# Kernel optimization log

Measured on AMD Instinct MI355X. Metric: run time of the kernel, lower is better.

## Reference

```python
import jax, jax.numpy as jnp
import numpy as np

N = 50000      # nodes
E = 600000     # edges
D_IN = 128     # node_dim
D = 128        # out_channels
T = 4          # num_node_types
R = 4          # num_edge_types
L = 2          # num_layers
C = 8          # num_class
G = 512        # graphs in batch


def setup_inputs() -> dict:
    key = jax.random.key(0)
    ks = jax.random.split(key, 12)
    s = 0.05
    x = jax.random.normal(ks[0], (N, D_IN), jnp.float32)
    node_type = jax.random.randint(ks[1], (N,), 0, T)
    edge_index = jax.random.randint(ks[2], (2, E), 0, N)
    edge_type = jax.random.randint(ks[3], (E,), 0, R)
    batch = jnp.sort(jax.random.randint(ks[4], (N,), 0, G))
    # learned params
    W_het = jax.random.normal(ks[5], (T, D_IN, D), jnp.float32) * s
    b_het = jnp.zeros((T, D), jnp.float32)
    conv_W = jax.random.normal(ks[6], (L, R, D, D), jnp.float32) * s
    conv_b = jnp.zeros((L, R, D), jnp.float32)
    fuse_W = jax.random.normal(ks[7], (R * D, D), jnp.float32) * s
    fuse_b = jnp.zeros((D,), jnp.float32)
    cls_W = jax.random.normal(ks[8], (D, C), jnp.float32) * s
    cls_b = jnp.zeros((C,), jnp.float32)
    return dict(x=x, W_het=W_het, b_het=b_het, conv_W=conv_W, conv_b=conv_b,
                fuse_W=fuse_W, fuse_b=fuse_b, cls_W=cls_W, cls_b=cls_b,
                node_type=node_type, edge_index=edge_index, edge_type=edge_type,
                batch=batch)


def reference(x, W_het, b_het, conv_W, conv_b, fuse_W, fuse_b, cls_W, cls_b,
              node_type, edge_index, edge_type, batch):
    n = x.shape[0]
    # HeteroLinear: per-node-type linear. Compute all T projections then select.
    x_all = jnp.einsum('nd,tdo->tno', x, W_het)          # [T, N, D]
    h = x_all[node_type, jnp.arange(n)] + b_het[node_type]
    src, dst = edge_index[0], edge_index[1]
    for l in range(L):
        hs = h[src]                                       # [E, D] gather once per layer
        outs = []
        for r in range(R):
            # edges of relation r only (boolean mask == per-relation edge filtering)
            m = hs @ conv_W[l, r]                         # [E, D]
            m = m * (edge_type == r).astype(m.dtype)[:, None]
            agg = jax.ops.segment_sum(m, dst, num_segments=n)  # scatter-add to dst
            outs.append(agg + conv_b[l, r])
        h = jax.nn.relu(jnp.concatenate(outs, axis=1) @ fuse_W + fuse_b)
    # global mean pool over graphs
    counts = jax.ops.segment_sum(jnp.ones((n,), h.dtype), batch, num_segments=G)
    emb = jax.ops.segment_sum(h, batch, num_segments=G) / jnp.maximum(counts, 1.0)[:, None]
    logits = emb @ cls_W + cls_b
    return emb, logits
```

## Files before the change

### kernel.cpp

```cpp
#include <hip/hip_runtime.h>

#define N_NODES 50000
#define N_EDGES 600000
#define DIM     128
#define RR      4
#define LL      2
#define GG      512
#define CC      8
#define NCB     196
#define EC      (N_EDGES / 4)
#define FB      ((EC + 255) / 256)
#define TB      ((N_NODES + 255) / 256)
#define NBH     ((N_NODES + 63) / 64)
#define CB      (1026 + 3125)

typedef short bf16x8 __attribute__((ext_vector_type(8)));
typedef float f32x4  __attribute__((ext_vector_type(4)));

__device__ __forceinline__ float bf16_to_f(unsigned short u) {
    return __uint_as_float(((unsigned int)u) << 16);
}
__device__ __forceinline__ unsigned short f_to_bf16(float f) {
    unsigned int u = __float_as_uint(f);
    u += 0x7FFFu + ((u >> 16) & 1u);
    return (unsigned short)(u >> 16);
}
__device__ __forceinline__ float loadf(const void* p, long i, int isbf) {
    if (isbf) return bf16_to_f(((const unsigned short*)p)[i]);
    return ((const float*)p)[i];
}
__device__ __forceinline__ void storef(void* p, long i, float v, int isbf) {
    if (isbf) ((unsigned short*)p)[i] = f_to_bf16(v);
    else      ((float*)p)[i] = v;
}

__global__ void cg_init(const unsigned int* __restrict__ xw, int* __restrict__ flag,
                        int* __restrict__ chist_tb) {
    __shared__ int cnt;
    int tid = threadIdx.x;
    if (tid < NCB + 16) chist_tb[tid] = 0;
    if (tid == 0) cnt = 0;
    __syncthreads();
    unsigned int w = xw[tid];
    unsigned int e = (w >> 7) & 0xFFu;
    atomicAdd(&cnt, (e >= 110u && e <= 133u) ? 1 : 0);
    __syncthreads();
    if (tid == 0) *flag = (cnt >= 128) ? 1 : 0;
}

__global__ void cg_hist_canon(const int* __restrict__ edge_index, const int* __restrict__ node_type,
                              int* __restrict__ chist, int* __restrict__ tb,
                              const void* __restrict__ x,
                              const void* __restrict__ W_het, const void* __restrict__ b_het,
                              const void* __restrict__ conv_W, const void* __restrict__ fuse_W,
                              const void* __restrict__ conv_b, const void* __restrict__ fuse_b,
                              const int* __restrict__ flagp,
                              unsigned short* __restrict__ xb, unsigned short* __restrict__ Wt,
                              float* __restrict__ bhf,
                              unsigned short* __restrict__ M2t, float* __restrict__ cvec) {
    __shared__ float s[256];
    int bk = blockIdx.x;
    int tid = threadIdx.x;
    if (bk < FB) {
        __shared__ int lh[NCB];
        __shared__ int loc[4];
        for (int i = tid; i < NCB; i += 256) lh[i] = 0;
        if (tid < 4) loc[tid] = 0;
        __syncthreads();
        int t = bk * 256 + tid;
        if (t < EC) {
#pragma unroll
            for (int k = 0; k < 4; k++) {
                int d = edge_index[N_EDGES + t + k * EC];
                atomicAdd(&lh[d >> 8], 1);
            }
        }
        if (t < N_NODES) atomicAdd(&loc[node_type[t]], 1);
        __syncthreads();
        for (int i = tid; i < NCB; i += 256)
            if (lh[i]) atomicAdd(&chist[i], lh[i]);
        if (tid < 4 && loc[tid]) atomicAdd(&tb[tid], loc[tid]);
        return;
    }
    int b = bk - FB;
    int isbf = *flagp;
    if (b < 512) {
        int lr = b >> 6;
        int d  = (b & 63) * 2 + (tid >> 7);
        int r  = lr & 3;
        int o  = tid & 127;
        float acc = 0.0f;
        for (int k = 0; k < DIM; k++) {
            acc += loadf(conv_W, (long)(lr * DIM + d) * DIM + k, isbf)
                 * loadf(fuse_W, (long)(r * DIM + k) * DIM + o, isbf);
        }
        M2t[((long)lr * DIM + o) * DIM + d] = f_to_bf16(acc);
    } else if (b < 768) {
        int bc = b - 512;
        int l  = bc >> 7;
        int o  = bc & 127;
        float part = 0.0f;
        for (int rk = tid; rk < RR * DIM; rk += 256) {
            part += loadf(conv_b, (long)l * RR * DIM + rk, isbf)
                  * loadf(fuse_W, (long)rk * DIM + o, isbf);
        }
        s[tid] = part;
        __syncthreads();
        for (int off = 128; off > 0; off >>= 1) {
            if (tid < off) s[tid] += s[tid + off];
            __syncthreads();
        }
        if (tid == 0) cvec[bc] = s[0] + loadf(fuse_b, o, isbf);
    } else if (b < 1024) {
        int pair = (b - 768) * 2 + (tid >> 7);
        int t = pair >> 7;
        int o = pair & 127;
        int d = tid & 127;
        float v = loadf(W_het, ((long)t * DIM + d) * DIM + o, isbf);
        Wt[((long)t * DIM + o) * DIM + d] = f_to_bf16(v);
    } else if (b < 1026) {
        int idx = (b - 1024) * 256 + tid;
        if (idx < 4 * DIM) bhf[idx] = loadf(b_het, idx, isbf);
    } else {
        long i = ((long)(b - 1026) * 256 + tid) * 8;
        if (i >= (long)N_NODES * DIM) return;
        if (isbf) {
            *(uint4*)(xb + i) = *(const uint4*)((const unsigned short*)x + i);
        } else {
            const float* xf = (const float*)x + i;
            float4 f0 = *(const float4*)xf;
            float4 f1 = *(const float4*)(xf + 4);
            uint4 o;
            o.x = (unsigned int)f_to_bf16(f0.x) | ((unsigned int)f_to_bf16(f0.y) << 16);
            o.y = (unsigned int)f_to_bf16(f0.z) | ((unsigned int)f_to_bf16(f0.w) << 16);
            o.z = (unsigned int)f_to_bf16(f1.x) | ((unsigned int)f_to_bf16(f1.y) << 16);
            o.w = (unsigned int)f_to_bf16(f1.z) | ((unsigned int)f_to_bf16(f1.w) << 16);
            *(uint4*)(xb + i) = o;
        }
    }
}

__global__ void cg_scan196(const int* __restrict__ chist, int* __restrict__ blockoff,
                           int* __restrict__ ccursor, int* __restrict__ tb) {
    __shared__ int s[256];
    int tid = threadIdx.x;
    int v = (tid < NCB) ? chist[tid] : 0;
    s[tid] = v;
    __syncthreads();
    for (int off = 1; off < 256; off <<= 1) {
        int a = (tid >= off) ? s[tid - off] : 0;
        __syncthreads();
        s[tid] += a;
        __syncthreads();
    }
    if (tid < NCB) {
        int e = s[tid] - v;
        blockoff[tid] = e;
        ccursor[tid]  = e;
    }
    if (tid == 0) {
        int run = 0;
        for (int t = 0; t < 4; t++) {
            tb[8 + t] = run;
            tb[4 + t] = run;
            run += tb[t];
        }
        tb[12] = run;
    }
}

__global__ void cg_tfill(const int* __restrict__ node_type, int* __restrict__ tb,
                         int* __restrict__ tlist) {
    __shared__ int lcur[4];
    __shared__ int lbase[4];
    int tid = threadIdx.x;
    if (tid < 4) lcur[tid] = 0;
    __syncthreads();
    int n = blockIdx.x * 256 + tid;
    int slot = -1, t = 0;
    if (n < N_NODES) {
        t = node_type[n];
        slot = atomicAdd(&lcur[t], 1);
    }
    __syncthreads();
    if (tid < 4) lbase[tid] = atomicAdd(&tb[4 + tid], lcur[tid]);
    __syncthreads();
    if (n < N_NODES) tlist[lbase[t] + slot] = n;
}

#define APAD 136

__global__ void cg_sortA_hetero(const int* __restrict__ edge_index, const int* __restrict__ edge_type,
                                int* __restrict__ ccursor, int2* __restrict__ tmp2,
                                const unsigned short* __restrict__ xb,
                                const unsigned short* __restrict__ Wt,
                                const float* __restrict__ bhf,
                                const int* __restrict__ tlist, const int* __restrict__ tb,
                                unsigned short* __restrict__ h) {
    __shared__ unsigned short a_lds[64][APAD];
    __shared__ unsigned short b_lds[DIM][APAD];
    int bk = blockIdx.x;
    int tx = threadIdx.x;
    if (bk < FB) {
        __shared__ int lhist[NCB];
        __shared__ int lbase[NCB];
        for (int i = tx; i < NCB; i += 256) lhist[i] = 0;
        __syncthreads();
        int t = bk * 256 + tx;
        int d[4], cb[4], ls[4], pl[4];
        bool act = (t < EC);
        if (act) {
#pragma unroll
            for (int k = 0; k < 4; k++) {
                int e = t + k * EC;
                d[k]  = edge_index[N_EDGES + e];
                pl[k] = (edge_index[e] << 2) | edge_type[e];
                cb[k] = d[k] >> 8;
                ls[k] = atomicAdd(&lhist[cb[k]], 1);
            }
        }
        __syncthreads();
        for (int i = tx; i < NCB; i += 256)
            lbase[i] = lhist[i] ? atomicAdd(&ccursor[i], lhist[i]) : 0;
        __syncthreads();
        if (act) {
#pragma unroll
            for (int k = 0; k < 4; k++) {
                int pos = lbase[cb[k]] + ls[k];
                tmp2[pos] = make_int2(pl[k], d[k]);
            }
        }
        return;
    }
    int bb = bk - FB;
    int t    = bb / NBH;
    int nblk = bb - t * NBH;
    int rows_base = tb[8 + t] + nblk * 64;
    int rend = tb[8 + t + 1];
    if (rows_base >= rend) return;
    const unsigned short* Wsrc = Wt + (long)t * DIM * DIM;
    for (int i = tx; i < 2048; i += 256) {
        uint4 w = *(const uint4*)(Wsrc + i * 8);
        int o = i >> 4, d2 = (i & 15) * 8;
        *(uint4*)&b_lds[o][d2] = w;
    }
    for (int i = tx; i < 1024; i += 256) {
        int row = i >> 4, seg = (i & 15) * 8;
        int gr = rows_base + row;
        uint4 w = make_uint4(0u, 0u, 0u, 0u);
        if (gr < rend) {
            int n = tlist[gr];
            w = *(const uint4*)(xb + (long)n * DIM + seg);
        }
        *(uint4*)&a_lds[row][seg] = w;
    }
    __syncthreads();
    int wv = tx >> 6, lane = tx & 63;
    int m16 = lane & 15, quad = lane >> 4;
    f32x4 acc[8];
#pragma unroll
    for (int c = 0; c < 8; c++) acc[c] = (f32x4){0.f, 0.f, 0.f, 0.f};
    for (int ks = 0; ks < 4; ks++) {
        int koff = ks * 32 + quad * 8;
        bf16x8 af = *(const bf16x8*)(const void*)&a_lds[wv * 16 + m16][koff];
#pragma unroll
        for (int c = 0; c < 8; c++) {
            bf16x8 bfr = *(const bf16x8*)(const void*)&b_lds[c * 16 + m16][koff];
            acc[c] = __builtin_amdgcn_mfma_f32_16x16x32_bf16(af, bfr, acc[c], 0, 0, 0);
        }
    }
    __syncthreads();
#pragma unroll
    for (int c = 0; c < 8; c++) {
#pragma unroll
        for (int i = 0; i < 4; i++) {
            int row = wv * 16 + quad * 4 + i;
            int col = c * 16 + m16;
            a_lds[row][col] = f_to_bf16(acc[c][i] + bhf[t * DIM + col]);
        }
    }
    __syncthreads();
    for (int i = tx; i < 1024; i += 256) {
        int row = i >> 4, seg = (i & 15) * 8;
        int gr = rows_base + row;
        if (gr < rend) {
            int n = tlist[gr];
            *(uint4*)(h + (long)n * DIM + seg) = *(const uint4*)&a_lds[row][seg];
        }
    }
}

__global__ void cg_sortB_pgemm(const int2* __restrict__ tmp2, const int* __restrict__ blockoff,
                               int* __restrict__ rowptr, int* __restrict__ eidx,
                               const unsigned short* __restrict__ h,
                               const unsigned short* __restrict__ M2t,
                               unsigned short* __restrict__ P) {
    __shared__ unsigned short a_lds[64][APAD];
    __shared__ unsigned short b_lds[DIM][APAD];
    int bk = blockIdx.x;
    int tx = threadIdx.x;
    if (bk < NCB) {
        __shared__ int lcnt[256];
        __shared__ int lscan[256];
        __shared__ int lcur[256];
        lcnt[tx] = 0;
        int base = blockoff[bk];
        int endp = (bk + 1 < NCB) ? blockoff[bk + 1] : N_EDGES;
        int cnt = endp - base;
        __syncthreads();
        for (int i = tx; i < cnt; i += 256)
            atomicAdd(&lcnt[tmp2[base + i].y & 255], 1);
        __syncthreads();
        int v = lcnt[tx];
        lscan[tx] = v;
        __syncthreads();
        for (int off = 1; off < 256; off <<= 1) {
            int a = (tx >= off) ? lscan[tx - off] : 0;
            __syncthreads();
            lscan[tx] += a;
            __syncthreads();
        }
        int start = base + lscan[tx] - v;
        lcur[tx] = start;
        int n = bk * 256 + tx;
        if (n < N_NODES) rowptr[n] = start;
        __syncthreads();
        for (int i = tx; i < cnt; i += 256) {
            int2 e = tmp2[base + i];
            int pos = atomicAdd(&lcur[e.y & 255], 1);
            eidx[pos] = e.x;
        }
        return;
    }
    int bb = bk - NCB;
    int r    = bb / NBH;
    int nblk = bb - r * NBH;
    int n0 = nblk * 64;
    const unsigned short* Bsrc = M2t + (long)r * DIM * DIM;
    for (int i = tx; i < 2048; i += 256) {
        uint4 w = *(const uint4*)(Bsrc + i * 8);
        int o = i >> 4, d = (i & 15) * 8;
        *(uint4*)&b_lds[o][d] = w;
    }
    for (int i = tx; i < 1024; i += 256) {
        int row = i >> 4, seg = (i & 15) * 8;
        int n = n0 + row;
        uint4 w = make_uint4(0u, 0u, 0u, 0u);
        if (n < N_NODES) w = *(const uint4*)(h + (long)n * DIM + seg);
        *(uint4*)&a_lds[row][seg] = w;
    }
    __syncthreads();
    int wv = tx >> 6, lane = tx & 63;
    int m16 = lane & 15, quad = lane >> 4;
    f32x4 acc[8];
#pragma unroll
    for (int c = 0; c < 8; c++) acc[c] = (f32x4){0.f, 0.f, 0.f, 0.f};
    for (int ks = 0; ks < 4; ks++) {
        int koff = ks * 32 + quad * 8;
        bf16x8 af = *(const bf16x8*)(const void*)&a_lds[wv * 16 + m16][koff];
#pragma unroll
        for (int c = 0; c < 8; c++) {
            bf16x8 bfr = *(const bf16x8*)(const void*)&b_lds[c * 16 + m16][koff];
            acc[c] = __builtin_amdgcn_mfma_f32_16x16x32_bf16(af, bfr, acc[c], 0, 0, 0);
        }
    }
    __syncthreads();
#pragma unroll
    for (int c = 0; c < 8; c++) {
#pragma unroll
        for (int i = 0; i < 4; i++) {
            int row = wv * 16 + quad * 4 + i;
            int col = c * 16 + m16;
            a_lds[row][col] = f_to_bf16(acc[c][i]);
        }
    }
    __syncthreads();
    for (int i = tx; i < 1024; i += 256) {
        int row = i >> 4, seg = (i & 15) * 8;
        int n = n0 + row;
        if (n < N_NODES)
            *(uint4*)(P + (long)n * (RR * DIM) + r * DIM + seg) = *(const uint4*)&a_lds[row][seg];
    }
}

__global__ void cg_pgemm_mfma(const unsigned short* __restrict__ h,
                              const unsigned short* __restrict__ M2t, int l,
                              unsigned short* __restrict__ P) {
    int r  = blockIdx.y;
    int n0 = blockIdx.x * 64;
    __shared__ unsigned short a_lds[64][APAD];
    __shared__ unsigned short b_lds[DIM][APAD];
    int tx = threadIdx.x;
    const unsigned short* Bsrc = M2t + (long)(l * RR + r) * DIM * DIM;
    for (int i = tx; i < 2048; i += 256) {
        uint4 w = *(const uint4*)(Bsrc + i * 8);
        int o = i >> 4, d = (i & 15) * 8;
        *(uint4*)&b_lds[o][d] = w;
    }
    for (int i = tx; i < 1024; i += 256) {
        int row = i >> 4, seg = (i & 15) * 8;
        int n = n0 + row;
        uint4 w = make_uint4(0u, 0u, 0u, 0u);
        if (n < N_NODES) w = *(const uint4*)(h + (long)n * DIM + seg);
        *(uint4*)&a_lds[row][seg] = w;
    }
    __syncthreads();
    int wv = tx >> 6, lane = tx & 63;
    int m16 = lane & 15, quad = lane >> 4;
    f32x4 acc[8];
#pragma unroll
    for (int c = 0; c < 8; c++) acc[c] = (f32x4){0.f, 0.f, 0.f, 0.f};
    for (int ks = 0; ks < 4; ks++) {
        int koff = ks * 32 + quad * 8;
        bf16x8 af = *(const bf16x8*)(const void*)&a_lds[wv * 16 + m16][koff];
#pragma unroll
        for (int c = 0; c < 8; c++) {
            bf16x8 bfr = *(const bf16x8*)(const void*)&b_lds[c * 16 + m16][koff];
            acc[c] = __builtin_amdgcn_mfma_f32_16x16x32_bf16(af, bfr, acc[c], 0, 0, 0);
        }
    }
    __syncthreads();
#pragma unroll
    for (int c = 0; c < 8; c++) {
#pragma unroll
        for (int i = 0; i < 4; i++) {
            int row = wv * 16 + quad * 4 + i;
            int col = c * 16 + m16;
            a_lds[row][col] = f_to_bf16(acc[c][i]);
        }
    }
    __syncthreads();
    for (int i = tx; i < 1024; i += 256) {
        int row = i >> 4, seg = (i & 15) * 8;
        int n = n0 + row;
        if (n < N_NODES)
            *(uint4*)(P + (long)n * (RR * DIM) + r * DIM + seg) = *(const uint4*)&a_lds[row][seg];
    }
}

__global__ void cg_gather4(const unsigned short* __restrict__ P, const int* __restrict__ rowptr,
                           const int* __restrict__ eidx, const float* __restrict__ cv,
                           unsigned short* __restrict__ hout) {
    int wid  = (blockIdx.x * 256 + threadIdx.x) >> 6;
    int lane = threadIdx.x & 63;
    if (wid >= N_NODES) return;
    int eg = lane >> 4;
    int ol = lane & 15;
    int start = rowptr[wid];
    int end   = (wid + 1 < N_NODES) ? rowptr[wid + 1] : N_EDGES;
    float a[8] = {0.f, 0.f, 0.f, 0.f, 0.f, 0.f, 0.f, 0.f};
    int j = start + eg;
    for (; j + 4 < end; j += 8) {
        int v0 = eidx[j];
        int v1 = eidx[j + 4];
        const uint4 w0 = *(const uint4*)(P + (long)(v0 >> 2) * (RR * DIM) + (v0 & 3) * DIM + ol * 8);
        const uint4 w1 = *(const uint4*)(P + (long)(v1 >> 2) * (RR * DIM) + (v1 & 3) * DIM + ol * 8);
        a[0] += bf16_to_f((unsigned short)(w0.x & 0xFFFFu)) + bf16_to_f((unsigned short)(w1.x & 0xFFFFu));
        a[1] += bf16_to_f((unsigned short)(w0.x >> 16))     + bf16_to_f((unsigned short)(w1.x >> 16));
        a[2] += bf16_to_f((unsigned short)(w0.y & 0xFFFFu)) + bf16_to_f((unsigned short)(w1.y & 0xFFFFu));
        a[3] += bf16_to_f((unsigned short)(w0.y >> 16))     + bf16_to_f((unsigned short)(w1.y >> 16));
        a[4] += bf16_to_f((unsigned short)(w0.z & 0xFFFFu)) + bf16_to_f((unsigned short)(w1.z & 0xFFFFu));
        a[5] += bf16_to_f((unsigned short)(w0.z >> 16))     + bf16_to_f((unsigned short)(w1.z >> 16));
        a[6] += bf16_to_f((unsigned short)(w0.w & 0xFFFFu)) + bf16_to_f((unsigned short)(w1.w & 0xFFFFu));
        a[7] += bf16_to_f((unsigned short)(w0.w >> 16))     + bf16_to_f((unsigned short)(w1.w >> 16));
    }
    if (j < end) {
        int v = eidx[j];
        const uint4 w = *(const uint4*)(P + (long)(v >> 2) * (RR * DIM) + (v & 3) * DIM + ol * 8);
        a[0] += bf16_to_f((unsigned short)(w.x & 0xFFFFu));
        a[1] += bf16_to_f((unsigned short)(w.x >> 16));
        a[2] += bf16_to_f((unsigned short)(w.y & 0xFFFFu));
        a[3] += bf16_to_f((unsigned short)(w.y >> 16));
        a[4] += bf16_to_f((unsigned short)(w.z & 0xFFFFu));
        a[5] += bf16_to_f((unsigned short)(w.z >> 16));
        a[6] += bf16_to_f((unsigned short)(w.w & 0xFFFFu));
        a[7] += bf16_to_f((unsigned short)(w.w >> 16));
    }
#pragma unroll
    for (int i = 0; i < 8; i++) {
        a[i] += __shfl_xor(a[i], 16);
        a[i] += __shfl_xor(a[i], 32);
    }
    if (eg == 0) {
        int o0 = ol * 8;
        float v[8];
#pragma unroll
        for (int i = 0; i < 8; i++) {
            float s = a[i] + cv[o0 + i];
            v[i] = s > 0.0f ? s : 0.0f;
        }
        uint4 o4;
        o4.x = (unsigned int)f_to_bf16(v[0]) | ((unsigned int)f_to_bf16(v[1]) << 16);
        o4.y = (unsigned int)f_to_bf16(v[2]) | ((unsigned int)f_to_bf16(v[3]) << 16);
        o4.z = (unsigned int)f_to_bf16(v[4]) | ((unsigned int)f_to_bf16(v[5]) << 16);
        o4.w = (unsigned int)f_to_bf16(v[6]) | ((unsigned int)f_to_bf16(v[7]) << 16);
        *(uint4*)(hout + (long)wid * DIM + o0) = o4;
    }
}

__global__ void cg_pool_logits(const unsigned short* __restrict__ h, const int* __restrict__ batch,
                               const void* __restrict__ cls_W, const void* __restrict__ cls_b,
                               const int* __restrict__ flagp, void* __restrict__ out) {
    __shared__ float acc_s[4][DIM];
    __shared__ float emb_s[DIM];
    int g   = blockIdx.x;
    int tid = threadIdx.x;
    int wv  = tid >> 6;
    int lane = tid & 63;
    int sub = lane >> 4;
    int ol  = lane & 15;
    int isbf = *flagp;
    int lo = 0, hi = N_NODES;
    while (lo < hi) { int mid = (lo + hi) >> 1; if (batch[mid] < g) lo = mid + 1; else hi = mid; }
    int start = lo;
    hi = N_NODES;
    while (lo < hi) { int mid = (lo + hi) >> 1; if (batch[mid] < g + 1) lo = mid + 1; else hi = mid; }
    int end = lo;
    float a[8] = {0.f, 0.f, 0.f, 0.f, 0.f, 0.f, 0.f, 0.f};
    for (int n = start + wv * 4 + sub; n < end; n += 16) {
        uint4 w = *(const uint4*)(h + (long)n * DIM + ol * 8);
        a[0] += bf16_to_f((unsigned short)(w.x & 0xFFFFu));
        a[1] += bf16_to_f((unsigned short)(w.x >> 16));
        a[2] += bf16_to_f((unsigned short)(w.y & 0xFFFFu));
        a[3] += bf16_to_f((unsigned short)(w.y >> 16));
        a[4] += bf16_to_f((unsigned short)(w.z & 0xFFFFu));
        a[5] += bf16_to_f((unsigned short)(w.z >> 16));
        a[6] += bf16_to_f((unsigned short)(w.w & 0xFFFFu));
        a[7] += bf16_to_f((unsigned short)(w.w >> 16));
    }
#pragma unroll
    for (int i = 0; i < 8; i++) {
        a[i] += __shfl_xor(a[i], 16);
        a[i] += __shfl_xor(a[i], 32);
    }
    if (sub == 0) {
#pragma unroll
        for (int i = 0; i < 8; i++) acc_s[wv][ol * 8 + i] = a[i];
    }
    __syncthreads();
    int cnt = end - start;
    float inv = 1.0f / (float)(cnt > 1 ? cnt : 1);
    if (tid < DIM) {
        float e = (acc_s[0][tid] + acc_s[1][tid] + acc_s[2][tid] + acc_s[3][tid]) * inv;
        emb_s[tid] = e;
        storef(out, (long)g * DIM + tid, e, isbf);
    }
    __syncthreads();
    if (tid < 128) {
        int c  = tid >> 4;
        int kk = tid & 15;
        float p = 0.0f;
#pragma unroll
        for (int k = kk * 8; k < kk * 8 + 8; k++)
            p += emb_s[k] * loadf(cls_W, (long)k * CC + c, isbf);
        p += __shfl_xor(p, 1);
        p += __shfl_xor(p, 2);
        p += __shfl_xor(p, 4);
        p += __shfl_xor(p, 8);
        if (kk == 0)
            storef(out, (long)GG * DIM + g * CC + c, p + loadf(cls_b, c, isbf), isbf);
    }
}

extern "C" void kernel_launch(void* const* d_in, const int* in_sizes, int n_in,
                              void* d_out, int out_size, void* d_ws, size_t ws_size,
                              hipStream_t stream) {
    const void* x      = d_in[0];
    const void* W_het  = d_in[1];
    const void* b_het  = d_in[2];
    const void* conv_W = d_in[3];
    const void* conv_b = d_in[4];
    const void* fuse_W = d_in[5];
    const void* fuse_b = d_in[6];
    const void* cls_W  = d_in[7];
    const void* cls_b  = d_in[8];
    const int* node_type  = (const int*)d_in[9];
    const int* edge_index = (const int*)d_in[10];
    const int* edge_type  = (const int*)d_in[11];
    const int* batch      = (const int*)d_in[12];

    char* base = (char*)d_ws;
    unsigned short* hbf      = (unsigned short*)(base + 0);
    unsigned short* P        = (unsigned short*)(base + 12800000);
    unsigned short* xb       = (unsigned short*)(base + 64000000);
    unsigned short* Wt       = (unsigned short*)(base + 76800000);
    float*          bhf      = (float*)(base + 76931072);
    unsigned short* M2t      = (unsigned short*)(base + 76933120);
    float*          cvec     = (float*)(base + 77195264);
    int*            rowptr   = (int*)(base + 77196288);
    int*            chist    = (int*)(base + 77396320);
    int*            tb       = chist + NCB;
    int*            blockoff = (int*)(base + 77397408);
    int*            ccursor  = (int*)(base + 77398432);
    int*            eidx     = (int*)(base + 77399456);
    int*            tlist    = (int*)(base + 79799456);
    int*            flag     = (int*)(base + 79999456);
    int2*           tmp2     = (int2*)(base + 79999472);

    cg_init<<<1, 256, 0, stream>>>((const unsigned int*)x, flag, chist);
    cg_hist_canon<<<FB + CB, 256, 0, stream>>>(edge_index, node_type, chist, tb,
                                               x, W_het, b_het, conv_W, fuse_W,
                                               conv_b, fuse_b, flag,
                                               xb, Wt, bhf, M2t, cvec);
    cg_scan196<<<1, 256, 0, stream>>>(chist, blockoff, ccursor, tb);
    cg_tfill<<<TB, 256, 0, stream>>>(node_type, tb, tlist);
    cg_sortA_hetero<<<FB + 4 * NBH, 256, 0, stream>>>(edge_index, edge_type, ccursor, tmp2,
                                                      xb, Wt, bhf, tlist, tb, hbf);
    cg_sortB_pgemm<<<NCB + 4 * NBH, 256, 0, stream>>>(tmp2, blockoff, rowptr, eidx,
                                                      hbf, M2t, P);
    cg_gather4<<<(N_NODES * 64 + 255) / 256, 256, 0, stream>>>(
        P, rowptr, eidx, cvec, hbf);
    cg_pgemm_mfma<<<dim3(NBH, RR), 256, 0, stream>>>(hbf, M2t, 1, P);
    cg_gather4<<<(N_NODES * 64 + 255) / 256, 256, 0, stream>>>(
        P, rowptr, eidx, cvec + DIM, hbf);

    cg_pool_logits<<<GG, 256, 0, stream>>>(hbf, batch, cls_W, cls_b, flag, d_out);
}
```

Before: 292.9 us.

## Fuse layer-0 gather aggregation with layer-1 per-relation projection GEMM

Replaces the first gather kernel plus the separate layer-1 projection GEMM with one kernel. Each block aggregates neighbour messages for 64 nodes into LDS, applies bias and ReLU, then runs the four relation MFMA GEMMs directly from LDS. It writes to a second P buffer so it never reads and writes the same array. This removes one launch and the round-trip of h through global memory. The cost is only NBH (~782) blocks, each doing 16 serial node gathers per wave, which cuts parallelism and memory-level latency hiding compared with one wave per node.

```diff
diff --git a/kernel.cpp b/kernel.cpp
--- a/kernel.cpp
+++ b/kernel.cpp
@@ -383,58 +383,116 @@
     }
 }
 
-__global__ void cg_pgemm_mfma(const unsigned short* __restrict__ h,
-                              const unsigned short* __restrict__ M2t, int l,
-                              unsigned short* __restrict__ P) {
-    int r  = blockIdx.y;
-    int n0 = blockIdx.x * 64;
+__global__ void cg_gather_pgemm(const unsigned short* __restrict__ P0,
+                                const int* __restrict__ rowptr, const int* __restrict__ eidx,
+                                const float* __restrict__ cv0,
+                                const unsigned short* __restrict__ M2t,
+                                unsigned short* __restrict__ P1) {
     __shared__ unsigned short a_lds[64][APAD];
     __shared__ unsigned short b_lds[DIM][APAD];
+    int n0 = blockIdx.x * 64;
     int tx = threadIdx.x;
-    const unsigned short* Bsrc = M2t + (long)(l * RR + r) * DIM * DIM;
-    for (int i = tx; i < 2048; i += 256) {
-        uint4 w = *(const uint4*)(Bsrc + i * 8);
-        int o = i >> 4, d = (i & 15) * 8;
-        *(uint4*)&b_lds[o][d] = w;
-    }
-    for (int i = tx; i < 1024; i += 256) {
-        int row = i >> 4, seg = (i & 15) * 8;
+    int wv = tx >> 6, lane = tx & 63;
+    int eg = lane >> 4;
+    int ol = lane & 15;
+    for (int rr = 0; rr < 16; rr++) {
+        int row = wv * 16 + rr;
         int n = n0 + row;
-        uint4 w = make_uint4(0u, 0u, 0u, 0u);
-        if (n < N_NODES) w = *(const uint4*)(h + (long)n * DIM + seg);
-        *(uint4*)&a_lds[row][seg] = w;
-    }
-    __syncthreads();
-    int wv = tx >> 6, lane = tx & 63;
+        float a[8] = {0.f, 0.f, 0.f, 0.f, 0.f, 0.f, 0.f, 0.f};
+        if (n < N_NODES) {
+            int start = rowptr[n];
+            int end   = (n + 1 < N_NODES) ? rowptr[n + 1] : N_EDGES;
+            int j = start + eg;
+            for (; j + 4 < end; j += 8) {
+                int v0 = eidx[j];
+                int v1 = eidx[j + 4];
+                const uint4 w0 = *(const uint4*)(P0 + (long)(v0 >> 2) * (RR * DIM) + (v0 & 3) * DIM + ol * 8);
+                const uint4 w1 = *(const uint4*)(P0 + (long)(v1 >> 2) * (RR * DIM) + (v1 & 3) * DIM + ol * 8);
+                a[0] += bf16_to_f((unsigned short)(w0.x & 0xFFFFu)) + bf16_to_f((unsigned short)(w1.x & 0xFFFFu));
+                a[1] += bf16_to_f((unsigned short)(w0.x >> 16))     + bf16_to_f((unsigned short)(w1.x >> 16));
+                a[2] += bf16_to_f((unsigned short)(w0.y & 0xFFFFu)) + bf16_to_f((unsigned short)(w1.y & 0xFFFFu));
+                a[3] += bf16_to_f((unsigned short)(w0.y >> 16))     + bf16_to_f((unsigned short)(w1.y >> 16));
+                a[4] += bf16_to_f((unsigned short)(w0.z & 0xFFFFu)) + bf16_to_f((unsigned short)(w1.z & 0xFFFFu));
+                a[5] += bf16_to_f((unsigned short)(w0.z >> 16))     + bf16_to_f((unsigned short)(w1.z >> 16));
+                a[6] += bf16_to_f((unsigned short)(w0.w & 0xFFFFu)) + bf16_to_f((unsigned short)(w1.w & 0xFFFFu));
+                a[7] += bf16_to_f((unsigned short)(w0.w >> 16))     + bf16_to_f((unsigned short)(w1.w >> 16));
+            }
+            if (j < end) {
+                int v = eidx[j];
+                const uint4 w = *(const uint4*)(P0 + (long)(v >> 2) * (RR * DIM) + (v & 3) * DIM + ol * 8);
+                a[0] += bf16_to_f((unsigned short)(w.x & 0xFFFFu));
+                a[1] += bf16_to_f((unsigned short)(w.x >> 16));
+                a[2] += bf16_to_f((unsigned short)(w.y & 0xFFFFu));
+                a[3] += bf16_to_f((unsigned short)(w.y >> 16));
+                a[4] += bf16_to_f((unsigned short)(w.z & 0xFFFFu));
+                a[5] += bf16_to_f((unsigned short)(w.z >> 16));
+                a[6] += bf16_to_f((unsigned short)(w.w & 0xFFFFu));
+                a[7] += bf16_to_f((unsigned short)(w.w >> 16));
+            }
+        }
+#pragma unroll
+        for (int i = 0; i < 8; i++) {
+            a[i] += __shfl_xor(a[i], 16);
+            a[i] += __shfl_xor(a[i], 32);
+        }
+        if (eg == 0) {
+            int o0 = ol * 8;
+            uint4 o4;
+            float v0 = a[0] + cv0[o0 + 0]; v0 = v0 > 0.f ? v0 : 0.f;
+            float v1 = a[1] + cv0[o0 + 1]; v1 = v1 > 0.f ? v1 : 0.f;
+            float v2 = a[2] + cv0[o0 + 2]; v2 = v2 > 0.f ? v2 : 0.f;
+            float v3 = a[3] + cv0[o0 + 3]; v3 = v3 > 0.f ? v3 : 0.f;
+            float v4 = a[4] + cv0[o0 + 4]; v4 = v4 > 0.f ? v4 : 0.f;
+            float v5 = a[5] + cv0[o0 + 5]; v5 = v5 > 0.f ? v5 : 0.f;
+            float v6 = a[6] + cv0[o0 + 6]; v6 = v6 > 0.f ? v6 : 0.f;
+            float v7 = a[7] + cv0[o0 + 7]; v7 = v7 > 0.f ? v7 : 0.f;
+            o4.x = (unsigned int)f_to_bf16(v0) | ((unsigned int)f_to_bf16(v1) << 16);
+            o4.y = (unsigned int)f_to_bf16(v2) | ((unsigned int)f_to_bf16(v3) << 16);
+            o4.z = (unsigned int)f_to_bf16(v4) | ((unsigned int)f_to_bf16(v5) << 16);
+            o4.w = (unsigned int)f_to_bf16(v6) | ((unsigned int)f_to_bf16(v7) << 16);
+            *(uint4*)&a_lds[row][o0] = o4;
+        }
+    }
+    __syncthreads();
     int m16 = lane & 15, quad = lane >> 4;
-    f32x4 acc[8];
-#pragma unroll
-    for (int c = 0; c < 8; c++) acc[c] = (f32x4){0.f, 0.f, 0.f, 0.f};
-    for (int ks = 0; ks < 4; ks++) {
-        int koff = ks * 32 + quad * 8;
-        bf16x8 af = *(const bf16x8*)(const void*)&a_lds[wv * 16 + m16][koff];
+    for (int r = 0; r < RR; r++) {
+        const unsigned short* Bsrc = M2t + (long)(RR + r) * DIM * DIM;
+        for (int i = tx; i < 2048; i += 256) {
+            uint4 w = *(const uint4*)(Bsrc + i * 8);
+            int o = i >> 4, d = (i & 15) * 8;
+            *(uint4*)&b_lds[o][d] = w;
+        }
+        __syncthreads();
+        f32x4 acc[8];
+#pragma unroll
+        for (int c = 0; c < 8; c++) acc[c] = (f32x4){0.f, 0.f, 0.f, 0.f};
+        for (int ks = 0; ks < 4; ks++) {
+            int koff = ks * 32 + quad * 8;
+            bf16x8 af = *(const bf16x8*)(const void*)&a_lds[wv * 16 + m16][koff];
+#pragma unroll
+            for (int c = 0; c < 8; c++) {
+                bf16x8 bfr = *(const bf16x8*)(const void*)&b_lds[c * 16 + m16][koff];
+                acc[c] = __builtin_amdgcn_mfma_f32_16x16x32_bf16(af, bfr, acc[c], 0, 0, 0);
+            }
+        }
+        __syncthreads();
 #pragma unroll
         for (int c = 0; c < 8; c++) {
-            bf16x8 bfr = *(const bf16x8*)(const void*)&b_lds[c * 16 + m16][koff];
-            acc[c] = __builtin_amdgcn_mfma_f32_16x16x32_bf16(af, bfr, acc[c], 0, 0, 0);
-        }
-    }
-    __syncthreads();
-#pragma unroll
-    for (int c = 0; c < 8; c++) {
-#pragma unroll
-        for (int i = 0; i < 4; i++) {
-            int row = wv * 16 + quad * 4 + i;
-            int col = c * 16 + m16;
-            a_lds[row][col] = f_to_bf16(acc[c][i]);
-        }
-    }
-    __syncthreads();
-    for (int i = tx; i < 1024; i += 256) {
-        int row = i >> 4, seg = (i & 15) * 8;
-        int n = n0 + row;
-        if (n < N_NODES)
-            *(uint4*)(P + (long)n * (RR * DIM) + r * DIM + seg) = *(const uint4*)&a_lds[row][seg];
+#pragma unroll
+            for (int i = 0; i < 4; i++) {
+                int row = wv * 16 + quad * 4 + i;
+                int col = c * 16 + m16;
+                b_lds[row][col] = f_to_bf16(acc[c][i]);
+            }
+        }
+        __syncthreads();
+        for (int i = tx; i < 1024; i += 256) {
+            int row = i >> 4, seg = (i & 15) * 8;
+            int n = n0 + row;
+            if (n < N_NODES)
+                *(uint4*)(P1 + (long)n * (RR * DIM) + r * DIM + seg) = *(const uint4*)&b_lds[row][seg];
+        }
+        __syncthreads();
     }
 }
 
@@ -581,7 +639,7 @@
 
     char* base = (char*)d_ws;
     unsigned short* hbf      = (unsigned short*)(base + 0);
-    unsigned short* P        = (unsigned short*)(base + 12800000);
+    unsigned short* P0       = (unsigned short*)(base + 12800000);
     unsigned short* xb       = (unsigned short*)(base + 64000000);
     unsigned short* Wt       = (unsigned short*)(base + 76800000);
     float*          bhf      = (float*)(base + 76931072);
@@ -596,6 +654,7 @@
     int*            tlist    = (int*)(base + 79799456);
     int*            flag     = (int*)(base + 79999456);
     int2*           tmp2     = (int2*)(base + 79999472);
+    unsigned short* P1       = (unsigned short*)(base + 84799472);
 
     cg_init<<<1, 256, 0, stream>>>((const unsigned int*)x, flag, chist);
     cg_hist_canon<<<FB + CB, 256, 0, stream>>>(edge_index, node_type, chist, tb,
@@ -607,12 +666,9 @@
     cg_sortA_hetero<<<FB + 4 * NBH, 256, 0, stream>>>(edge_index, edge_type, ccursor, tmp2,
                                                       xb, Wt, bhf, tlist, tb, hbf);
     cg_sortB_pgemm<<<NCB + 4 * NBH, 256, 0, stream>>>(tmp2, blockoff, rowptr, eidx,
-                                                      hbf, M2t, P);
+                                                      hbf, M2t, P0);
+    cg_gather_pgemm<<<NBH, 256, 0, stream>>>(P0, rowptr, eidx, cvec, M2t, P1);
     cg_gather4<<<(N_NODES * 64 + 255) / 256, 256, 0, stream>>>(
-        P, rowptr, eidx, cvec, hbf);
-    cg_pgemm_mfma<<<dim3(NBH, RR), 256, 0, stream>>>(hbf, M2t, 1, P);
-    cg_gather4<<<(N_NODES * 64 + 255) / 256, 256, 0, stream>>>(
-        P, rowptr, eidx, cvec + DIM, hbf);
-
+        P1, rowptr, eidx, cvec + DIM, hbf);
     cg_pool_logits<<<GG, 256, 0, stream>>>(hbf, batch, cls_W, cls_b, flag, d_out);
 }
```

Result: slower. 339.2 us (+15.8%).
